# Performance work log

Hardware: AMD Instinct MI355X
Metric: run time of the kernel (lower is better)

## Reference

```python
import jax, jax.numpy as jnp
import numpy as np

N, E, B, D, L, IN, H = 50000, 800000, 64, 64, 4, 7, 4


def _leaky(x, s=0.2):
    return jnp.where(x >= 0, x, s * x)


def _layernorm(x, g, b, eps=1e-5):
    mu = x.mean(-1, keepdims=True)
    v = ((x - mu) ** 2).mean(-1, keepdims=True)
    return (x - mu) * jax.lax.rsqrt(v + eps) * g + b


def _forward(x, edge_index, batch,
             enc_W, enc_b,
             gat_Wl, gat_Wr, gat_att, gat_b,
             ln_g, ln_b, ffn_W1, ffn_b1, ffn_W2, ffn_b2,
             n2g_W1, n2g_b1, n2g_W2, n2g_b2,
             g2n_W1, g2n_b1, g2n_W2, g2n_b2,
             dec_W1, dec_b1, dec_W2, dec_b2):
    n = x.shape[0]
    loops = jnp.arange(n, dtype=edge_index.dtype)
    src = jnp.concatenate([edge_index[0], loops])  # PyG add_self_loops=True
    dst = jnp.concatenate([edge_index[1], loops])

    h = x @ enc_W + enc_b  # encoder [N, D]
    for l in range(L):
        # ---- GATv2Conv(heads=4, concat=False), eval mode (dropout off) ----
        xl = (h @ gat_Wl[l]).reshape(n, H, D)  # source transform (lin_l)
        xr = (h @ gat_Wr[l]).reshape(n, H, D)  # target transform (lin_r)
        s = xl[src] + xr[dst]                              # [Et, H, D]
        e = jnp.sum(_leaky(s) * gat_att[l], axis=-1)       # [Et, H]
        m = jax.ops.segment_max(e, dst, num_segments=n)
        a = jnp.exp(e - m[dst])
        denom = jax.ops.segment_sum(a, dst, num_segments=n)
        a = a / (denom[dst] + 1e-16)                       # segment softmax
        out = jax.ops.segment_sum(a[..., None] * xl[src], dst, num_segments=n)
        out = out.mean(axis=1) + gat_b[l]                  # head average + bias
        # ---- residual + LayerNorm + FFN ----
        h2 = _layernorm(h + out, ln_g[l], ln_b[l])
        h = h2 + (_leaky(h2 @ ffn_W1[l] + ffn_b1[l]) @ ffn_W2[l] + ffn_b2[l])
        # ---- GlobalContextLayer ----
        lat = jax.nn.gelu(h @ n2g_W1[l] + n2g_b1[l]) @ n2g_W2[l] + n2g_b2[l]
        cnt = jax.ops.segment_sum(jnp.ones((n, 1), h.dtype), batch, num_segments=B)
        gmean = jax.ops.segment_sum(lat, batch, num_segments=B) / jnp.maximum(cnt, 1.0)
        gmax = jax.ops.segment_max(lat, batch, num_segments=B)
        gl = jnp.concatenate([gmean, gmax], axis=1)        # [B, 2D]
        ctx = jax.nn.gelu(gl @ g2n_W1[l] + g2n_b1[l]) @ g2n_W2[l] + g2n_b2[l]
        h = h + ctx[batch]
    return jax.nn.gelu(h @ dec_W1 + dec_b1) @ dec_W2 + dec_b2  # [N, 2]


def setup_inputs() -> dict:
    key = jax.random.key(0)
    ks = jax.random.split(key, 16)
    f = lambda i, s: jax.random.normal(ks[i], s, dtype=jnp.float32) * 0.1
    z = lambda s: jnp.zeros(s, jnp.float32)
    return dict(
        x=jax.random.normal(ks[0], (N, IN), dtype=jnp.float32),
        edge_index=jax.random.randint(ks[1], (2, E), 0, N, dtype=jnp.int32),
        batch=jnp.sort(jax.random.randint(ks[2], (N,), 0, B, dtype=jnp.int32)),
        enc_W=f(3, (IN, D)), enc_b=z((D,)),
        gat_Wl=f(4, (L, D, H * D)), gat_Wr=f(5, (L, D, H * D)),
        gat_att=f(6, (L, H, D)), gat_b=z((L, D)),
        ln_g=jnp.ones((L, D), jnp.float32), ln_b=z((L, D)),
        ffn_W1=f(7, (L, D, 2 * D)), ffn_b1=z((L, 2 * D)),
        ffn_W2=f(8, (L, 2 * D, D)), ffn_b2=z((L, D)),
        n2g_W1=f(9, (L, D, D)), n2g_b1=z((L, D)),
        n2g_W2=f(10, (L, D, D)), n2g_b2=z((L, D)),
        g2n_W1=f(11, (L, 2 * D, D)), g2n_b1=z((L, D)),
        g2n_W2=f(12, (L, D, D)), g2n_b2=z((L, D)),
        dec_W1=f(13, (D, D)), dec_b1=z((D,)),
        dec_W2=f(14, (D, 2)), dec_b2=z((2,)),
    )


def reference(x, edge_index, batch, enc_W, enc_b, gat_Wl, gat_Wr, gat_att, gat_b,
              ln_g, ln_b, ffn_W1, ffn_b1, ffn_W2, ffn_b2,
              n2g_W1, n2g_b1, n2g_W2, n2g_b2,
              g2n_W1, g2n_b1, g2n_W2, g2n_b2,
              dec_W1, dec_b1, dec_W2, dec_b2):
    return _forward(x, edge_index, batch, enc_W, enc_b, gat_Wl, gat_Wr, gat_att, gat_b,
                    ln_g, ln_b, ffn_W1, ffn_b1, ffn_W2, ffn_b2,
                    n2g_W1, n2g_b1, n2g_W2, n2g_b2,
                    g2n_W1, g2n_b1, g2n_W2, g2n_b2,
                    dec_W1, dec_b1, dec_W2, dec_b2)
```

## Files before the change

### kernel.cpp

```cpp
#include <hip/hip_runtime.h>
#include <hip/hip_bf16.h>
#include <math.h>

#define NN 50000
#define EE 800000
#define BBATCH 64
#define DDIM 64
#define NLAYER 4
#define NIN 7
#define NHEAD 4

typedef __attribute__((ext_vector_type(8))) short short8v;
typedef __attribute__((ext_vector_type(4))) float f32x4;

static __device__ __forceinline__ float wave_sum(float v) {
#pragma unroll
  for (int m = 32; m > 0; m >>= 1) v += __shfl_xor(v, m, 64);
  return v;
}

static __device__ __forceinline__ float gelu_t(float x) {
  float z = 0.7978845608f * (x + 0.044715f * x * x * x);
  float t = 2.f / (1.f + __expf(-2.f * z)) - 1.f;
  return 0.5f * x * (1.f + t);
}

static __device__ __forceinline__ unsigned short f2b(float v) {
  __hip_bfloat16 b = __float2bfloat16(v);
  return *reinterpret_cast<unsigned short*>(&b);
}

static __device__ __forceinline__ float b2f(unsigned short u) {
  return __builtin_bit_cast(float, (unsigned int)u << 16);
}

template <int CTRL>
static __device__ __forceinline__ float dppf(float v) {
  int x = __builtin_amdgcn_mov_dpp(__builtin_bit_cast(int, v), CTRL, 0xF, 0xF, true);
  return __builtin_bit_cast(float, x);
}

static __device__ __forceinline__ void unpack8(uint4 u, float* xs) {
  unsigned int w[4] = {u.x, u.y, u.z, u.w};
#pragma unroll
  for (int k = 0; k < 4; k++) {
    xs[2 * k]     = __builtin_bit_cast(float, w[k] << 16);
    xs[2 * k + 1] = __builtin_bit_cast(float, w[k] & 0xFFFF0000u);
  }
}

__global__ void k_init_cnt(int* cnt, int n) {
  int i = blockIdx.x * blockDim.x + threadIdx.x;
  if (i < n) cnt[i] = 1;
}

__global__ void k_count_edges(const int* __restrict__ dst, int e, int* cnt) {
  int i = blockIdx.x * blockDim.x + threadIdx.x;
  if (i < e) atomicAdd(&cnt[dst[i]], 1);
}

__global__ void k_scan_bsum(const int* __restrict__ cnt, int n, int* bsum) {
  __shared__ int red[256];
  int b = blockIdx.x, t = threadIdx.x;
  int s = 0;
  for (int i = b * 1024 + t; i < (b + 1) * 1024; i += 256)
    if (i < n) s += cnt[i];
  red[t] = s;
  __syncthreads();
  for (int o = 128; o > 0; o >>= 1) {
    if (t < o) red[t] += red[t + o];
    __syncthreads();
  }
  if (t == 0) bsum[b] = red[0];
}

__global__ void k_scan_offsets(int* bsum, int nb) {
  if (threadIdx.x == 0 && blockIdx.x == 0) {
    int acc = 0;
    for (int i = 0; i < nb; i++) { int v = bsum[i]; bsum[i] = acc; acc += v; }
  }
}

__global__ void k_scan_final(const int* __restrict__ cnt, int n,
                             const int* __restrict__ bsum, int* indptr) {
  __shared__ int lds[256];
  int b = blockIdx.x, t = threadIdx.x;
  int base = b * 1024;
  int v[4];
  int s = 0;
#pragma unroll
  for (int j = 0; j < 4; j++) {
    int i = base + t * 4 + j;
    v[j] = (i < n) ? cnt[i] : 0;
    s += v[j];
  }
  lds[t] = s;
  __syncthreads();
  for (int o = 1; o < 256; o <<= 1) {
    int x = (t >= o) ? lds[t - o] : 0;
    __syncthreads();
    lds[t] += x;
    __syncthreads();
  }
  int run = bsum[b] + lds[t] - s;
#pragma unroll
  for (int j = 0; j < 4; j++) {
    int i = base + t * 4 + j;
    if (i <= n) indptr[i] = run;
    run += v[j];
  }
}

__global__ void k_csr_self(const int* __restrict__ indptr, int* nxt, int* esrc, int n) {
  int i = blockIdx.x * blockDim.x + threadIdx.x;
  if (i < n) {
    int p = indptr[i];
    esrc[p] = i;
    nxt[i] = p + 1;
  }
}

__global__ void k_csr_fill(const int* __restrict__ src, const int* __restrict__ dst,
                           int e, int* nxt, int* esrc) {
  int i = blockIdx.x * blockDim.x + threadIdx.x;
  if (i < e) {
    int p = atomicAdd(&nxt[dst[i]], 1);
    esrc[p] = src[i];
  }
}

__global__ void k_batch_starts(const int* __restrict__ batch, int n, int nb, int* starts) {
  int i = blockIdx.x * blockDim.x + threadIdx.x;
  if (i >= n) return;
  int b = batch[i];
  if (i == 0) {
    for (int x = 0; x <= b; x++) starts[x] = 0;
  } else {
    int pb = batch[i - 1];
    if (pb != b)
      for (int x = pb + 1; x <= b; x++) starts[x] = i;
  }
  if (i == n - 1) {
    for (int x = b + 1; x <= nb; x++) starts[x] = n;
  }
}

#define SEG_LR (4 * 512 * 64)
#define SEG_F1 (4 * 128 * 64)
#define SEG_F2 (4 * 64 * 128)
#define SEG_N  (4 * 64 * 64)
#define SEG_D  (64 * 64)
#define WPREP_TOTAL (SEG_LR + SEG_F1 + SEG_F2 + 2 * SEG_N + SEG_D)
__global__ void k_wprep_all(const float* __restrict__ Wl, const float* __restrict__ Wr,
                            const float* __restrict__ F1, const float* __restrict__ F2,
                            const float* __restrict__ N1, const float* __restrict__ N2,
                            const float* __restrict__ D1,
                            unsigned short* __restrict__ wLR, unsigned short* __restrict__ wF1,
                            unsigned short* __restrict__ wF2, unsigned short* __restrict__ wN1,
                            unsigned short* __restrict__ wN2, unsigned short* __restrict__ wD1) {
  int idx = blockIdx.x * blockDim.x + threadIdx.x;
  if (idx < SEG_LR) {
    int l = idx / (512 * 64), rem = idx % (512 * 64);
    int c = rem / 64, k = rem % 64;
    float v = (c < 256) ? Wl[(size_t)l * 64 * 256 + k * 256 + c]
                        : Wr[(size_t)l * 64 * 256 + k * 256 + (c - 256)];
    wLR[idx] = f2b(v);
    return;
  }
  idx -= SEG_LR;
  if (idx < SEG_F1) {
    int l = idx / (128 * 64), rem = idx % (128 * 64);
    int c = rem / 64, k = rem % 64;
    wF1[idx] = f2b(F1[(size_t)l * 64 * 128 + k * 128 + c]);
    return;
  }
  idx -= SEG_F1;
  if (idx < SEG_F2) {
    int l = idx / (64 * 128), rem = idx % (64 * 128);
    int c = rem / 128, k = rem % 128;
    wF2[idx] = f2b(F2[(size_t)l * 128 * 64 + k * 64 + c]);
    return;
  }
  idx -= SEG_F2;
  if (idx < SEG_N) {
    int l = idx / (64 * 64), rem = idx % (64 * 64);
    int c = rem / 64, k = rem % 64;
    wN1[idx] = f2b(N1[(size_t)l * 64 * 64 + k * 64 + c]);
    return;
  }
  idx -= SEG_N;
  if (idx < SEG_N) {
    int l = idx / (64 * 64), rem = idx % (64 * 64);
    int c = rem / 64, k = rem % 64;
    wN2[idx] = f2b(N2[(size_t)l * 64 * 64 + k * 64 + c]);
    return;
  }
  idx -= SEG_N;
  if (idx < SEG_D) {
    int c = idx / 64, k = idx % 64;
    wD1[idx] = f2b(D1[k * 64 + c]);
  }
}

__global__ void k_encoder(const float* __restrict__ x, const float* __restrict__ W,
                          const float* __restrict__ bias, float* __restrict__ h,
                          unsigned short* __restrict__ hb, int n) {
  int idx = blockIdx.x * blockDim.x + threadIdx.x;
  if (idx >= n * 64) return;
  int i = idx >> 6, d = idx & 63;
  float acc = bias[d];
#pragma unroll
  for (int k = 0; k < NIN; k++) acc += x[i * NIN + k] * W[k * 64 + d];
  h[idx] = acc;
  hb[idx] = f2b(acc);
}

template <int K, int ACT, bool RES, bool BIAS, bool OUTF, bool OUTB>
__global__ __launch_bounds__(256) void k_mgemm(const unsigned short* __restrict__ A,
                                               const unsigned short* __restrict__ Wt,
                                               const float* __restrict__ bias,
                                               const float* __restrict__ res,
                                               float* __restrict__ C,
                                               unsigned short* __restrict__ Cb,
                                               int n, int Co) {
  constexpr int NF = K / 32;
  const int lane = threadIdx.x & 63, wave = threadIdx.x >> 6;
  const int row0 = blockIdx.x * 64 + wave * 16;
  const int c0 = blockIdx.y * 64;
  const int karow = (lane >> 4) * 8;
  const int arow = row0 + (lane & 15);
  const size_t abase = (size_t)(arow < n ? arow : 0) * K + karow;

  short8v a[NF];
#pragma unroll
  for (int f = 0; f < NF; f++)
    a[f] = *(const short8v*)(A + abase + f * 32);

  f32x4 acc[4];
#pragma unroll
  for (int cc = 0; cc < 4; cc++) {
    const int c = c0 + cc * 16 + (lane & 15);
    f32x4 t = {0.f, 0.f, 0.f, 0.f};
#pragma unroll
    for (int f = 0; f < NF; f++) {
      short8v b = *(const short8v*)(Wt + (size_t)c * K + f * 32 + karow);
      t = __builtin_amdgcn_mfma_f32_16x16x32_bf16(a[f], b, t, 0, 0, 0);
    }
    acc[cc] = t;
  }

#pragma unroll
  for (int cc = 0; cc < 4; cc++) {
    const int c = c0 + cc * 16 + (lane & 15);
    const float bv = BIAS ? bias[c] : 0.f;
#pragma unroll
    for (int r = 0; r < 4; r++) {
      const int row = row0 + (lane >> 4) * 4 + r;
      if (row < n) {
        float v = acc[cc][r] + bv;
        if (ACT == 1) v = fmaxf(v, 0.2f * v);
        else if (ACT == 2) v = gelu_t(v);
        if (RES) v += res[(size_t)row * Co + c];
        if (OUTF) C[(size_t)row * Co + c] = v;
        if (OUTB) Cb[(size_t)row * Co + c] = f2b(v);
      }
    }
  }
}

__global__ __launch_bounds__(256) void k_gat(const unsigned short* __restrict__ xlr,
                                             const float* __restrict__ att,
                                             const float* __restrict__ gbias,
                                             const float* __restrict__ lng,
                                             const float* __restrict__ lnb,
                                             const float* __restrict__ h,
                                             const int* __restrict__ indptr,
                                             const int* __restrict__ esrc,
                                             float* __restrict__ h2,
                                             unsigned short* __restrict__ h2b, int n) {
  const int wave = threadIdx.x >> 6, lane = threadIdx.x & 63;
  const int node = blockIdx.x * 4 + wave;
  if (node >= n) return;
  const int q = lane >> 4, r = lane & 15;
  const int c = r & 3;
  const int doff = (r >> 2) * 64 + c * 16;

  float xr_d[16], att_d[16];
  {
    const uint4* xp = (const uint4*)(xlr + (size_t)node * 512 + 256 + doff);
    uint4 u0 = xp[0], u1 = xp[1];
    unpack8(u0, xr_d);
    unpack8(u1, xr_d + 8);
    const float4* ap = (const float4*)(att + doff);
#pragma unroll
    for (int k = 0; k < 4; k++) {
      float4 a = ap[k];
      att_d[4 * k] = a.x; att_d[4 * k + 1] = a.y;
      att_d[4 * k + 2] = a.z; att_d[4 * k + 3] = a.w;
    }
  }

  float acc[16] = {};
  float den = 0.f;
  const int beg = indptr[node], end = indptr[node + 1];

  int j0 = beg + q;
  bool valid = j0 < end;
  {
    int s0 = esrc[valid ? j0 : beg];
    const uint4* xp0 = (const uint4*)(xlr + (size_t)s0 * 512 + doff);
    uint4 u0 = xp0[0], u1 = xp0[1];

    for (int jb = beg; jb < end; jb += 4) {
      const uint4 cu0 = u0, cu1 = u1;
      const bool cvalid = valid;
      if (jb + 4 < end) {
        const int jn = jb + 4 + q;
        valid = jn < end;
        int sn = esrc[valid ? jn : beg];
        const uint4* xpn = (const uint4*)(xlr + (size_t)sn * 512 + doff);
        u0 = xpn[0];
        u1 = xpn[1];
      }
      float xs[16];
      unpack8(cu0, xs);
      unpack8(cu1, xs + 8);
      float p0 = 0.f, p1 = 0.f, p2 = 0.f, p3 = 0.f;
#pragma unroll
      for (int k = 0; k < 4; k++) {
        float t0 = xs[4 * k + 0] + xr_d[4 * k + 0]; t0 = fmaxf(t0, 0.2f * t0); p0 = fmaf(t0, att_d[4 * k + 0], p0);
        float t1 = xs[4 * k + 1] + xr_d[4 * k + 1]; t1 = fmaxf(t1, 0.2f * t1); p1 = fmaf(t1, att_d[4 * k + 1], p1);
        float t2 = xs[4 * k + 2] + xr_d[4 * k + 2]; t2 = fmaxf(t2, 0.2f * t2); p2 = fmaf(t2, att_d[4 * k + 2], p2);
        float t3 = xs[4 * k + 3] + xr_d[4 * k + 3]; t3 = fmaxf(t3, 0.2f * t3); p3 = fmaf(t3, att_d[4 * k + 3], p3);
      }
      float p = (p0 + p1) + (p2 + p3);
      p += dppf<0xB1>(p);
      p += dppf<0x4E>(p);
      const float pw = cvalid ? __expf(fminf(p, 60.f)) : 0.f;
      den += pw;
#pragma unroll
      for (int d = 0; d < 16; d++) acc[d] = fmaf(pw, xs[d], acc[d]);
    }
  }

  den += __shfl_xor(den, 16, 64);
  den += __shfl_xor(den, 32, 64);
#pragma unroll
  for (int d = 0; d < 16; d++) {
    acc[d] += __shfl_xor(acc[d], 16, 64);
    acc[d] += __shfl_xor(acc[d], 32, 64);
  }

  const float rden = 0.25f / (den + 1e-16f);
  float y[16];
  float s4 = 0.f;
  const float4* hp = (const float4*)(h + (size_t)node * 64 + c * 16);
  const float4* gp = (const float4*)(gbias + c * 16);
#pragma unroll
  for (int k = 0; k < 4; k++) {
    float4 hv = hp[k], gv = gp[k];
    float hf[4] = {hv.x, hv.y, hv.z, hv.w};
    float gf[4] = {gv.x, gv.y, gv.z, gv.w};
#pragma unroll
    for (int d2 = 0; d2 < 4; d2++) {
      int d = 4 * k + d2;
      float v = acc[d] * rden;
      v += dppf<0x124>(v);
      v += dppf<0x128>(v);
      y[d] = hf[d2] + v + gf[d2];
      s4 += y[d];
    }
  }

  const float mu = wave_sum(s4) * (1.f / 1024.f);
  float v4 = 0.f;
  float dv[16];
#pragma unroll
  for (int d = 0; d < 16; d++) {
    dv[d] = y[d] - mu;
    v4 += dv[d] * dv[d];
  }
  const float var = wave_sum(v4) * (1.f / 1024.f);
  const float rstd = rsqrtf(var + 1e-5f);

  if (lane < 4) {
    float4* outp = (float4*)(h2 + (size_t)node * 64 + lane * 16);
    uint2* outb = (uint2*)(h2b + (size_t)node * 64 + lane * 16);
    const float4* lgp = (const float4*)(lng + lane * 16);
    const float4* lbp = (const float4*)(lnb + lane * 16);
#pragma unroll
    for (int k = 0; k < 4; k++) {
      float4 g = lgp[k], b = lbp[k];
      float o0 = dv[4 * k + 0] * rstd * g.x + b.x;
      float o1 = dv[4 * k + 1] * rstd * g.y + b.y;
      float o2 = dv[4 * k + 2] * rstd * g.z + b.z;
      float o3 = dv[4 * k + 3] * rstd * g.w + b.w;
      float4 of; of.x = o0; of.y = o1; of.z = o2; of.w = o3;
      outp[k] = of;
      uint2 pk;
      pk.x = (unsigned int)f2b(o0) | ((unsigned int)f2b(o1) << 16);
      pk.y = (unsigned int)f2b(o2) | ((unsigned int)f2b(o3) << 16);
      outb[k] = pk;
    }
  }
}

__global__ void k_pool_part(const float* __restrict__ lat, const int* __restrict__ starts,
                            float* __restrict__ psum, float* __restrict__ pmax) {
  int b = blockIdx.x, p = blockIdx.y;
  int t = threadIdx.x;
  int lane = t & 63, sub = t >> 6;
  int s = starts[b], e = starts[b + 1];
  float sum = 0.f, mx = -3.4e38f;
  for (int i = s + p * 4 + sub; i < e; i += 32) {
    float v = lat[(size_t)i * 64 + lane];
    sum += v;
    mx = fmaxf(mx, v);
  }
  __shared__ float ls[4][64], lm[4][64];
  ls[sub][lane] = sum;
  lm[sub][lane] = mx;
  __syncthreads();
  if (sub == 0) {
#pragma unroll
    for (int j = 1; j < 4; j++) {
      sum += ls[j][lane];
      mx = fmaxf(mx, lm[j][lane]);
    }
    psum[(b * 8 + p) * 64 + lane] = sum;
    pmax[(b * 8 + p) * 64 + lane] = mx;
  }
}

__global__ void k_ctx2(const float* __restrict__ psum, const float* __restrict__ pmax,
                       const int* __restrict__ starts,
                       const float* __restrict__ W1, const float* __restrict__ b1,
                       const float* __restrict__ W2, const float* __restrict__ b2,
                       float* __restrict__ ctx) {
  int b = blockIdx.x;
  int t = threadIdx.x;
  __shared__ float g[128], tt[64];
  int cnt = starts[b + 1] - starts[b];
  if (t < 64) {
    float sm = 0.f;
#pragma unroll
    for (int p = 0; p < 8; p++) sm += psum[(b * 8 + p) * 64 + t];
    g[t] = sm / fmaxf((float)cnt, 1.0f);
  } else {
    float mx = -3.4e38f;
#pragma unroll
    for (int p = 0; p < 8; p++) mx = fmaxf(mx, pmax[(b * 8 + p) * 64 + (t - 64)]);
    g[t] = mx;
  }
  __syncthreads();
  if (t < 64) {
    float acc = b1[t];
    for (int k = 0; k < 128; k++) acc += g[k] * W1[k * 64 + t];
    tt[t] = gelu_t(acc);
  }
  __syncthreads();
  if (t < 64) {
    float acc2 = b2[t];
    for (int k = 0; k < 64; k++) acc2 += tt[k] * W2[k * 64 + t];
    ctx[b * 64 + t] = acc2;
  }
}

__global__ void k_add_ctx(float* __restrict__ h, unsigned short* __restrict__ hb,
                          const float* __restrict__ ctx,
                          const int* __restrict__ batch, int n) {
  int idx = blockIdx.x * blockDim.x + threadIdx.x;
  if (idx >= n * 64) return;
  int i = idx >> 6, d = idx & 63;
  float v = h[idx] + ctx[batch[i] * 64 + d];
  h[idx] = v;
  hb[idx] = f2b(v);
}

__global__ void k_dec2(const unsigned short* __restrict__ tD, const float* __restrict__ W2,
                       const float* __restrict__ b2, float* __restrict__ out, int n) {
  int i = blockIdx.x * blockDim.x + threadIdx.x;
  if (i >= n) return;
  const uint4* rp = (const uint4*)(tD + (size_t)i * 64);
  float a0 = b2[0], a1 = b2[1];
#pragma unroll
  for (int cblk = 0; cblk < 8; cblk++) {
    uint4 u = rp[cblk];
    float xs[8];
    unpack8(u, xs);
#pragma unroll
    for (int d = 0; d < 8; d++) {
      int k = cblk * 8 + d;
      a0 = fmaf(xs[d], W2[k * 2 + 0], a0);
      a1 = fmaf(xs[d], W2[k * 2 + 1], a1);
    }
  }
  out[2 * i] = a0;
  out[2 * i + 1] = a1;
}

extern "C" void kernel_launch(void* const* d_in, const int* in_sizes, int n_in,
                              void* d_out, int out_size, void* d_ws, size_t ws_size,
                              hipStream_t stream) {
  const float* x = (const float*)d_in[0];
  const int* ei = (const int*)d_in[1];
  const int* batch = (const int*)d_in[2];
  const float* enc_W = (const float*)d_in[3];
  const float* enc_b = (const float*)d_in[4];
  const float* gat_Wl = (const float*)d_in[5];
  const float* gat_Wr = (const float*)d_in[6];
  const float* gat_att = (const float*)d_in[7];
  const float* gat_b = (const float*)d_in[8];
  const float* ln_g = (const float*)d_in[9];
  const float* ln_b = (const float*)d_in[10];
  const float* ffn_W1 = (const float*)d_in[11];
  const float* ffn_b1 = (const float*)d_in[12];
  const float* ffn_W2 = (const float*)d_in[13];
  const float* ffn_b2 = (const float*)d_in[14];
  const float* n2g_W1 = (const float*)d_in[15];
  const float* n2g_b1 = (const float*)d_in[16];
  const float* n2g_W2 = (const float*)d_in[17];
  const float* n2g_b2 = (const float*)d_in[18];
  const float* g2n_W1 = (const float*)d_in[19];
  const float* g2n_b1 = (const float*)d_in[20];
  const float* g2n_W2 = (const float*)d_in[21];
  const float* g2n_b2 = (const float*)d_in[22];
  const float* dec_W1 = (const float*)d_in[23];
  const float* dec_b1 = (const float*)d_in[24];
  const float* dec_W2 = (const float*)d_in[25];
  const float* dec_b2 = (const float*)d_in[26];

  const int N = NN, E = EE;
  const int* e_src = ei;
  const int* e_dst = ei + E;

  float* h = (float*)d_ws;
  float* h2 = h + (size_t)N * 64;
  float* t1 = h2 + (size_t)N * 64;
  float* ctx = t1 + (size_t)N * 128;
  float* psum = ctx + BBATCH * 64;
  float* pmax = psum + BBATCH * 8 * 64;
  int* cnt = (int*)(pmax + BBATCH * 8 * 64);
  int* indptr = cnt + N;
  int* esrc = indptr + N + 1;
  int* bsum = esrc + (E + N);
  int* starts = bsum + 64;
  size_t off = (size_t)(starts + BBATCH + 1) - (size_t)d_ws;
  off = (off + 15) & ~(size_t)15;
  unsigned short* hb = (unsigned short*)((char*)d_ws + off);
  unsigned short* h2b = hb + (size_t)N * 64;
  unsigned short* tb = h2b + (size_t)N * 64;
  unsigned short* xlr = tb + (size_t)N * 128;
  unsigned short* wLR = xlr + (size_t)N * 512;
  unsigned short* wF1 = wLR + SEG_LR;
  unsigned short* wF2 = wF1 + SEG_F1;
  unsigned short* wN1 = wF2 + SEG_F2;
  unsigned short* wN2 = wN1 + SEG_N;
  unsigned short* wD1 = wN2 + SEG_N;

  float* lat = t1 + (size_t)N * 64;

  const int TPB = 256;
  const int NBLK_SCAN = (N + 1 + 1023) / 1024;

  hipLaunchKernelGGL(k_wprep_all, dim3((WPREP_TOTAL + 255) / 256), dim3(256), 0, stream,
                     gat_Wl, gat_Wr, ffn_W1, ffn_W2, n2g_W1, n2g_W2, dec_W1,
                     wLR, wF1, wF2, wN1, wN2, wD1);

  hipLaunchKernelGGL(k_init_cnt, dim3((N + TPB - 1) / TPB), dim3(TPB), 0, stream, cnt, N);
  hipLaunchKernelGGL(k_count_edges, dim3((E + TPB - 1) / TPB), dim3(TPB), 0, stream, e_dst, E, cnt);
  hipLaunchKernelGGL(k_scan_bsum, dim3(NBLK_SCAN), dim3(256), 0, stream, cnt, N, bsum);
  hipLaunchKernelGGL(k_scan_offsets, dim3(1), dim3(64), 0, stream, bsum, NBLK_SCAN);
  hipLaunchKernelGGL(k_scan_final, dim3(NBLK_SCAN), dim3(256), 0, stream, cnt, N, bsum, indptr);
  hipLaunchKernelGGL(k_csr_self, dim3((N + TPB - 1) / TPB), dim3(TPB), 0, stream, indptr, cnt, esrc, N);
  hipLaunchKernelGGL(k_csr_fill, dim3((E + TPB - 1) / TPB), dim3(TPB), 0, stream, e_src, e_dst, E, cnt, esrc);
  hipLaunchKernelGGL(k_batch_starts, dim3((N + TPB - 1) / TPB), dim3(TPB), 0, stream, batch, N, BBATCH, starts);

  hipLaunchKernelGGL(k_encoder, dim3((N * 64 + TPB - 1) / TPB), dim3(TPB), 0, stream,
                     x, enc_W, enc_b, h, hb, N);

  const int GN = (N + 63) / 64;

  for (int l = 0; l < NLAYER; l++) {
    const unsigned short* LRt = wLR + (size_t)l * 512 * 64;
    const unsigned short* F1t = wF1 + (size_t)l * 128 * 64;
    const unsigned short* F2t = wF2 + (size_t)l * 64 * 128;
    const unsigned short* N1t = wN1 + (size_t)l * 64 * 64;
    const unsigned short* N2t = wN2 + (size_t)l * 64 * 64;
    const float* attl = gat_att + (size_t)l * 256;
    const float* gbl = gat_b + (size_t)l * 64;
    const float* lngl = ln_g + (size_t)l * 64;
    const float* lnbl = ln_b + (size_t)l * 64;
    const float* fb1 = ffn_b1 + (size_t)l * 128;
    const float* fb2 = ffn_b2 + (size_t)l * 64;
    const float* nb1 = n2g_b1 + (size_t)l * 64;
    const float* nb2 = n2g_b2 + (size_t)l * 64;
    const float* gW1 = g2n_W1 + (size_t)l * 128 * 64;
    const float* gb1 = g2n_b1 + (size_t)l * 64;
    const float* gW2 = g2n_W2 + (size_t)l * 64 * 64;
    const float* gb2 = g2n_b2 + (size_t)l * 64;

    hipLaunchKernelGGL((k_mgemm<64, 0, false, false, false, true>), dim3(GN, 8), dim3(256), 0, stream,
                       hb, LRt, nullptr, nullptr, nullptr, xlr, N, 512);
    hipLaunchKernelGGL(k_gat, dim3((N + 3) / 4), dim3(256), 0, stream,
                       xlr, attl, gbl, lngl, lnbl, h, indptr, esrc, h2, h2b, N);
    hipLaunchKernelGGL((k_mgemm<64, 1, false, true, false, true>), dim3(GN, 2), dim3(256), 0, stream,
                       h2b, F1t, fb1, nullptr, nullptr, tb, N, 128);
    hipLaunchKernelGGL((k_mgemm<128, 0, true, true, true, true>), dim3(GN, 1), dim3(256), 0, stream,
                       tb, F2t, fb2, h2, h, hb, N, 64);
    hipLaunchKernelGGL((k_mgemm<64, 2, false, true, false, true>), dim3(GN, 1), dim3(256), 0, stream,
                       hb, N1t, nb1, nullptr, nullptr, tb, N, 64);
    hipLaunchKernelGGL((k_mgemm<64, 0, false, true, true, false>), dim3(GN, 1), dim3(256), 0, stream,
                       tb, N2t, nb2, nullptr, lat, nullptr, N, 64);
    hipLaunchKernelGGL(k_pool_part, dim3(BBATCH, 8), dim3(256), 0, stream,
                       lat, starts, psum, pmax);
    hipLaunchKernelGGL(k_ctx2, dim3(BBATCH), dim3(128), 0, stream,
                       psum, pmax, starts, gW1, gb1, gW2, gb2, ctx);
    hipLaunchKernelGGL(k_add_ctx, dim3((N * 64 + TPB - 1) / TPB), dim3(TPB), 0, stream,
                       h, hb, ctx, batch, N);
  }

  hipLaunchKernelGGL((k_mgemm<64, 2, false, true, false, true>), dim3(GN, 1), dim3(256), 0, stream,
                     hb, wD1, dec_b1, nullptr, nullptr, tb, N, 64);
  hipLaunchKernelGGL(k_dec2, dim3((N + TPB - 1) / TPB), dim3(TPB), 0, stream,
                     tb, dec_W2, dec_b2, (float*)d_out, N);
}
```

Baseline: 943.4 us.

## Fuse FFN, node-to-graph MLP with pooling, and decoder into single MFMA kernels

```diff
diff --git a/kernel.cpp b/kernel.cpp
--- a/kernel.cpp
+++ b/kernel.cpp
@@ -30,8 +30,13 @@
   return *reinterpret_cast<unsigned short*>(&b);
 }
 
-static __device__ __forceinline__ float b2f(unsigned short u) {
-  return __builtin_bit_cast(float, (unsigned int)u << 16);
+static __device__ __forceinline__ unsigned fkey(float x) {
+  unsigned u = __builtin_bit_cast(unsigned, x);
+  return (u >> 31) ? ~u : (u | 0x80000000u);
+}
+static __device__ __forceinline__ float fkey_inv(unsigned k) {
+  unsigned u = (k & 0x80000000u) ? (k ^ 0x80000000u) : ~k;
+  return __builtin_bit_cast(float, u);
 }
 
 template <int CTRL>
@@ -268,6 +273,152 @@
   }
 }
 
+__global__ __launch_bounds__(256) void k_ffn(const unsigned short* __restrict__ A,
+                                             const unsigned short* __restrict__ W1t,
+                                             const float* __restrict__ b1,
+                                             const unsigned short* __restrict__ W2t,
+                                             const float* __restrict__ b2,
+                                             const float* __restrict__ res,
+                                             float* __restrict__ C,
+                                             unsigned short* __restrict__ Cb, int n) {
+  __shared__ unsigned short tl[4][16 * 136];
+  const int lane = threadIdx.x & 63, wave = threadIdx.x >> 6;
+  const int row0 = blockIdx.x * 64 + wave * 16;
+  const int karow = (lane >> 4) * 8;
+  const int arow = row0 + (lane & 15);
+  const size_t abase = (size_t)(arow < n ? arow : 0) * 64 + karow;
+  short8v a0 = *(const short8v*)(A + abase);
+  short8v a1 = *(const short8v*)(A + abase + 32);
+
+#pragma unroll
+  for (int cc = 0; cc < 8; cc++) {
+    const int c = cc * 16 + (lane & 15);
+    f32x4 t = {0.f, 0.f, 0.f, 0.f};
+    t = __builtin_amdgcn_mfma_f32_16x16x32_bf16(a0, *(const short8v*)(W1t + (size_t)c * 64 + karow), t, 0, 0, 0);
+    t = __builtin_amdgcn_mfma_f32_16x16x32_bf16(a1, *(const short8v*)(W1t + (size_t)c * 64 + 32 + karow), t, 0, 0, 0);
+    const float bv = b1[c];
+#pragma unroll
+    for (int r = 0; r < 4; r++) {
+      float v = t[r] + bv;
+      v = fmaxf(v, 0.2f * v);
+      int rr = (lane >> 4) * 4 + r;
+      tl[wave][rr * 136 + c] = f2b(v);
+    }
+  }
+  __syncthreads();
+
+  short8v a2[4];
+#pragma unroll
+  for (int f = 0; f < 4; f++)
+    a2[f] = *(const short8v*)(&tl[wave][(lane & 15) * 136 + f * 32 + karow]);
+
+#pragma unroll
+  for (int cc = 0; cc < 4; cc++) {
+    const int c = cc * 16 + (lane & 15);
+    f32x4 t = {0.f, 0.f, 0.f, 0.f};
+#pragma unroll
+    for (int f = 0; f < 4; f++)
+      t = __builtin_amdgcn_mfma_f32_16x16x32_bf16(a2[f], *(const short8v*)(W2t + (size_t)c * 128 + f * 32 + karow), t, 0, 0, 0);
+    const float bv = b2[c];
+#pragma unroll
+    for (int r = 0; r < 4; r++) {
+      const int row = row0 + (lane >> 4) * 4 + r;
+      if (row < n) {
+        float v = t[r] + bv + res[(size_t)row * 64 + c];
+        C[(size_t)row * 64 + c] = v;
+        Cb[(size_t)row * 64 + c] = f2b(v);
+      }
+    }
+  }
+}
+
+__global__ __launch_bounds__(256) void k_n2g(const unsigned short* __restrict__ A,
+                                             const unsigned short* __restrict__ W1t,
+                                             const float* __restrict__ b1,
+                                             const unsigned short* __restrict__ W2t,
+                                             const float* __restrict__ b2,
+                                             const int* __restrict__ batch,
+                                             float* __restrict__ psum,
+                                             unsigned int* __restrict__ pmax, int n) {
+  __shared__ unsigned short tl[4][16 * 72];
+  __shared__ float s_sum[64];
+  __shared__ unsigned s_max[64];
+  const int lane = threadIdx.x & 63, wave = threadIdx.x >> 6;
+  const int row0b = blockIdx.x * 64;
+  const int row0 = row0b + wave * 16;
+  const int karow = (lane >> 4) * 8;
+  const int arow = row0 + (lane & 15);
+  const size_t abase = (size_t)(arow < n ? arow : 0) * 64 + karow;
+  if (threadIdx.x < 64) { s_sum[threadIdx.x] = 0.f; s_max[threadIdx.x] = 0u; }
+  short8v a0 = *(const short8v*)(A + abase);
+  short8v a1 = *(const short8v*)(A + abase + 32);
+
+#pragma unroll
+  for (int cc = 0; cc < 4; cc++) {
+    const int c = cc * 16 + (lane & 15);
+    f32x4 t = {0.f, 0.f, 0.f, 0.f};
+    t = __builtin_amdgcn_mfma_f32_16x16x32_bf16(a0, *(const short8v*)(W1t + (size_t)c * 64 + karow), t, 0, 0, 0);
+    t = __builtin_amdgcn_mfma_f32_16x16x32_bf16(a1, *(const short8v*)(W1t + (size_t)c * 64 + 32 + karow), t, 0, 0, 0);
+    const float bv = b1[c];
+#pragma unroll
+    for (int r = 0; r < 4; r++) {
+      int rr = (lane >> 4) * 4 + r;
+      tl[wave][rr * 72 + c] = f2b(gelu_t(t[r] + bv));
+    }
+  }
+  __syncthreads();
+
+  short8v a2[2];
+#pragma unroll
+  for (int f = 0; f < 2; f++)
+    a2[f] = *(const short8v*)(&tl[wave][(lane & 15) * 72 + f * 32 + karow]);
+
+  float pv[4][4];
+#pragma unroll
+  for (int cc = 0; cc < 4; cc++) {
+    const int c = cc * 16 + (lane & 15);
+    f32x4 t = {0.f, 0.f, 0.f, 0.f};
+    t = __builtin_amdgcn_mfma_f32_16x16x32_bf16(a2[0], *(const short8v*)(W2t + (size_t)c * 64 + karow), t, 0, 0, 0);
+    t = __builtin_amdgcn_mfma_f32_16x16x32_bf16(a2[1], *(const short8v*)(W2t + (size_t)c * 64 + 32 + karow), t, 0, 0, 0);
+    const float bv = b2[c];
+#pragma unroll
+    for (int r = 0; r < 4; r++) pv[cc][r] = t[r] + bv;
+  }
+
+  const int blo = batch[row0b];
+  const int last = row0b + 63 < n ? row0b + 63 : n - 1;
+  const int bhi = batch[last];
+  if (blo == bhi && row0b + 63 < n) {
+#pragma unroll
+    for (int cc = 0; cc < 4; cc++) {
+      const int c = cc * 16 + (lane & 15);
+      float s = pv[cc][0] + pv[cc][1] + pv[cc][2] + pv[cc][3];
+      float mx = fmaxf(fmaxf(pv[cc][0], pv[cc][1]), fmaxf(pv[cc][2], pv[cc][3]));
+      atomicAdd(&s_sum[c], s);
+      atomicMax(&s_max[c], fkey(mx));
+    }
+    __syncthreads();
+    if (threadIdx.x < 64) {
+      atomicAdd(&psum[blo * 64 + threadIdx.x], s_sum[threadIdx.x]);
+      atomicMax(&pmax[blo * 64 + threadIdx.x], s_max[threadIdx.x]);
+    }
+  } else {
+#pragma unroll
+    for (int cc = 0; cc < 4; cc++) {
+      const int c = cc * 16 + (lane & 15);
+#pragma unroll
+      for (int r = 0; r < 4; r++) {
+        const int row = row0 + (lane >> 4) * 4 + r;
+        if (row < n) {
+          const int b = batch[row];
+          atomicAdd(&psum[b * 64 + c], pv[cc][r]);
+          atomicMax(&pmax[b * 64 + c], fkey(pv[cc][r]));
+        }
+      }
+    }
+  }
+}
+
 __global__ __launch_bounds__(256) void k_gat(const unsigned short* __restrict__ xlr,
                                              const float* __restrict__ att,
                                              const float* __restrict__ gbias,
@@ -305,42 +456,42 @@
   const int beg = indptr[node], end = indptr[node + 1];
 
   int j0 = beg + q;
-  bool valid = j0 < end;
-  {
-    int s0 = esrc[valid ? j0 : beg];
-    const uint4* xp0 = (const uint4*)(xlr + (size_t)s0 * 512 + doff);
-    uint4 u0 = xp0[0], u1 = xp0[1];
-
-    for (int jb = beg; jb < end; jb += 4) {
-      const uint4 cu0 = u0, cu1 = u1;
-      const bool cvalid = valid;
-      if (jb + 4 < end) {
-        const int jn = jb + 4 + q;
-        valid = jn < end;
-        int sn = esrc[valid ? jn : beg];
-        const uint4* xpn = (const uint4*)(xlr + (size_t)sn * 512 + doff);
-        u0 = xpn[0];
-        u1 = xpn[1];
+  int s_cur = esrc[(j0 < end) ? j0 : beg];
+  const uint4* xp0 = (const uint4*)(xlr + (size_t)s_cur * 512 + doff);
+  uint4 u0 = xp0[0], u1 = xp0[1];
+  int jn1 = beg + 4 + q;
+  int s_nxt = esrc[(jn1 < end && beg + 4 < end) ? jn1 : beg];
+
+  for (int jb = beg; jb < end; jb += 4) {
+    const uint4 cu0 = u0, cu1 = u1;
+    const bool cvalid = (jb + q) < end;
+    if (jb + 4 < end) {
+      const uint4* xpn = (const uint4*)(xlr + (size_t)s_nxt * 512 + doff);
+      u0 = xpn[0];
+      u1 = xpn[1];
+      if (jb + 8 < end) {
+        const int jn = jb + 8 + q;
+        s_nxt = esrc[(jn < end) ? jn : beg];
       }
-      float xs[16];
-      unpack8(cu0, xs);
-      unpack8(cu1, xs + 8);
-      float p0 = 0.f, p1 = 0.f, p2 = 0.f, p3 = 0.f;
-#pragma unroll
-      for (int k = 0; k < 4; k++) {
-        float t0 = xs[4 * k + 0] + xr_d[4 * k + 0]; t0 = fmaxf(t0, 0.2f * t0); p0 = fmaf(t0, att_d[4 * k + 0], p0);
-        float t1 = xs[4 * k + 1] + xr_d[4 * k + 1]; t1 = fmaxf(t1, 0.2f * t1); p1 = fmaf(t1, att_d[4 * k + 1], p1);
-        float t2 = xs[4 * k + 2] + xr_d[4 * k + 2]; t2 = fmaxf(t2, 0.2f * t2); p2 = fmaf(t2, att_d[4 * k + 2], p2);
-        float t3 = xs[4 * k + 3] + xr_d[4 * k + 3]; t3 = fmaxf(t3, 0.2f * t3); p3 = fmaf(t3, att_d[4 * k + 3], p3);
-      }
-      float p = (p0 + p1) + (p2 + p3);
-      p += dppf<0xB1>(p);
-      p += dppf<0x4E>(p);
-      const float pw = cvalid ? __expf(fminf(p, 60.f)) : 0.f;
-      den += pw;
-#pragma unroll
-      for (int d = 0; d < 16; d++) acc[d] = fmaf(pw, xs[d], acc[d]);
-    }
+    }
+    float xs[16];
+    unpack8(cu0, xs);
+    unpack8(cu1, xs + 8);
+    float p0 = 0.f, p1 = 0.f, p2 = 0.f, p3 = 0.f;
+#pragma unroll
+    for (int k = 0; k < 4; k++) {
+      float t0 = xs[4 * k + 0] + xr_d[4 * k + 0]; t0 = fmaxf(t0, 0.2f * t0); p0 = fmaf(t0, att_d[4 * k + 0], p0);
+      float t1 = xs[4 * k + 1] + xr_d[4 * k + 1]; t1 = fmaxf(t1, 0.2f * t1); p1 = fmaf(t1, att_d[4 * k + 1], p1);
+      float t2 = xs[4 * k + 2] + xr_d[4 * k + 2]; t2 = fmaxf(t2, 0.2f * t2); p2 = fmaf(t2, att_d[4 * k + 2], p2);
+      float t3 = xs[4 * k + 3] + xr_d[4 * k + 3]; t3 = fmaxf(t3, 0.2f * t3); p3 = fmaf(t3, att_d[4 * k + 3], p3);
+    }
+    float p = (p0 + p1) + (p2 + p3);
+    p += dppf<0xB1>(p);
+    p += dppf<0x4E>(p);
+    const float pw = cvalid ? __expf(fminf(p, 60.f)) : 0.f;
+    den += pw;
+#pragma unroll
+    for (int d = 0; d < 16; d++) acc[d] = fmaf(pw, xs[d], acc[d]);
   }
 
   den += __shfl_xor(den, 16, 64);
@@ -405,34 +556,7 @@
   }
 }
 
-__global__ void k_pool_part(const float* __restrict__ lat, const int* __restrict__ starts,
-                            float* __restrict__ psum, float* __restrict__ pmax) {
-  int b = blockIdx.x, p = blockIdx.y;
-  int t = threadIdx.x;
-  int lane = t & 63, sub = t >> 6;
-  int s = starts[b], e = starts[b + 1];
-  float sum = 0.f, mx = -3.4e38f;
-  for (int i = s + p * 4 + sub; i < e; i += 32) {
-    float v = lat[(size_t)i * 64 + lane];
-    sum += v;
-    mx = fmaxf(mx, v);
-  }
-  __shared__ float ls[4][64], lm[4][64];
-  ls[sub][lane] = sum;
-  lm[sub][lane] = mx;
-  __syncthreads();
-  if (sub == 0) {
-#pragma unroll
-    for (int j = 1; j < 4; j++) {
-      sum += ls[j][lane];
-      mx = fmaxf(mx, lm[j][lane]);
-    }
-    psum[(b * 8 + p) * 64 + lane] = sum;
-    pmax[(b * 8 + p) * 64 + lane] = mx;
-  }
-}
-
-__global__ void k_ctx2(const float* __restrict__ psum, const float* __restrict__ pmax,
+__global__ void k_ctx2(const float* __restrict__ psum, const unsigned int* __restrict__ pmax,
                        const int* __restrict__ starts,
                        const float* __restrict__ W1, const float* __restrict__ b1,
                        const float* __restrict__ W2, const float* __restrict__ b2,
@@ -442,15 +566,9 @@
   __shared__ float g[128], tt[64];
   int cnt = starts[b + 1] - starts[b];
   if (t < 64) {
-    float sm = 0.f;
-#pragma unroll
-    for (int p = 0; p < 8; p++) sm += psum[(b * 8 + p) * 64 + t];
-    g[t] = sm / fmaxf((float)cnt, 1.0f);
+    g[t] = psum[b * 64 + t] / fmaxf((float)cnt, 1.0f);
   } else {
-    float mx = -3.4e38f;
-#pragma unroll
-    for (int p = 0; p < 8; p++) mx = fmaxf(mx, pmax[(b * 8 + p) * 64 + (t - 64)]);
-    g[t] = mx;
+    g[t] = fkey_inv(pmax[b * 64 + (t - 64)]);
   }
   __syncthreads();
   if (t < 64) {
@@ -477,26 +595,54 @@
   hb[idx] = f2b(v);
 }
 
-__global__ void k_dec2(const unsigned short* __restrict__ tD, const float* __restrict__ W2,
-                       const float* __restrict__ b2, float* __restrict__ out, int n) {
-  int i = blockIdx.x * blockDim.x + threadIdx.x;
-  if (i >= n) return;
-  const uint4* rp = (const uint4*)(tD + (size_t)i * 64);
-  float a0 = b2[0], a1 = b2[1];
-#pragma unroll
-  for (int cblk = 0; cblk < 8; cblk++) {
-    uint4 u = rp[cblk];
-    float xs[8];
-    unpack8(u, xs);
-#pragma unroll
-    for (int d = 0; d < 8; d++) {
-      int k = cblk * 8 + d;
-      a0 = fmaf(xs[d], W2[k * 2 + 0], a0);
-      a1 = fmaf(xs[d], W2[k * 2 + 1], a1);
-    }
-  }
-  out[2 * i] = a0;
-  out[2 * i + 1] = a1;
+__global__ __launch_bounds__(256) void k_dec(const unsigned short* __restrict__ A,
+                                             const unsigned short* __restrict__ W1t,
+                                             const float* __restrict__ b1,
+                                             const float* __restrict__ W2,
+                                             const float* __restrict__ b2,
+                                             float* __restrict__ out, int n) {
+  const int lane = threadIdx.x & 63, wave = threadIdx.x >> 6;
+  const int row0 = blockIdx.x * 64 + wave * 16;
+  const int karow = (lane >> 4) * 8;
+  const int arow = row0 + (lane & 15);
+  const size_t abase = (size_t)(arow < n ? arow : 0) * 64 + karow;
+  short8v a0 = *(const short8v*)(A + abase);
+  short8v a1 = *(const short8v*)(A + abase + 32);
+
+  float o0[4] = {}, o1[4] = {};
+#pragma unroll
+  for (int cc = 0; cc < 4; cc++) {
+    const int cidx = cc * 16 + (lane & 15);
+    f32x4 t = {0.f, 0.f, 0.f, 0.f};
+    t = __builtin_amdgcn_mfma_f32_16x16x32_bf16(a0, *(const short8v*)(W1t + (size_t)cidx * 64 + karow), t, 0, 0, 0);
+    t = __builtin_amdgcn_mfma_f32_16x16x32_bf16(a1, *(const short8v*)(W1t + (size_t)cidx * 64 + 32 + karow), t, 0, 0, 0);
+    const float bv = b1[cidx];
+    const float w0 = W2[cidx * 2 + 0], w1 = W2[cidx * 2 + 1];
+#pragma unroll
+    for (int r = 0; r < 4; r++) {
+      float v = gelu_t(t[r] + bv);
+      o0[r] = fmaf(v, w0, o0[r]);
+      o1[r] = fmaf(v, w1, o1[r]);
+    }
+  }
+#pragma unroll
+  for (int m = 1; m < 16; m <<= 1) {
+#pragma unroll
+    for (int r = 0; r < 4; r++) {
+      o0[r] += __shfl_xor(o0[r], m, 64);
+      o1[r] += __shfl_xor(o1[r], m, 64);
+    }
+  }
+  if ((lane & 15) == 0) {
+#pragma unroll
+    for (int r = 0; r < 4; r++) {
+      const int row = row0 + (lane >> 4) * 4 + r;
+      if (row < n) {
+        out[2 * row] = o0[r] + b2[0];
+        out[2 * row + 1] = o1[r] + b2[1];
+      }
+    }
+  }
 }
 
 extern "C" void kernel_launch(void* const* d_in, const int* in_sizes, int n_in,
@@ -536,11 +682,10 @@
 
   float* h = (float*)d_ws;
   float* h2 = h + (size_t)N * 64;
-  float* t1 = h2 + (size_t)N * 64;
-  float* ctx = t1 + (size_t)N * 128;
+  float* ctx = h2 + (size_t)N * 64;
   float* psum = ctx + BBATCH * 64;
-  float* pmax = psum + BBATCH * 8 * 64;
-  int* cnt = (int*)(pmax + BBATCH * 8 * 64);
+  unsigned int* pmax = (unsigned int*)(psum + BBATCH * 64);
+  int* cnt = (int*)(pmax + BBATCH * 64);
   int* indptr = cnt + N;
   int* esrc = indptr + N + 1;
   int* bsum = esrc + (E + N);
@@ -549,16 +694,13 @@
   off = (off + 15) & ~(size_t)15;
   unsigned short* hb = (unsigned short*)((char*)d_ws + off);
   unsigned short* h2b = hb + (size_t)N * 64;
-  unsigned short* tb = h2b + (size_t)N * 64;
-  unsigned short* xlr = tb + (size_t)N * 128;
+  unsigned short* xlr = h2b + (size_t)N * 64;
   unsigned short* wLR = xlr + (size_t)N * 512;
   unsigned short* wF1 = wLR + SEG_LR;
   unsigned short* wF2 = wF1 + SEG_F1;
   unsigned short* wN1 = wF2 + SEG_F2;
   unsigned short* wN2 = wN1 + SEG_N;
   unsigned short* wD1 = wN2 + SEG_N;
-
-  float* lat = t1 + (size_t)N * 64;
 
   const int TPB = 256;
   const int NBLK_SCAN = (N + 1 + 1023) / 1024;
@@ -604,24 +746,17 @@
                        hb, LRt, nullptr, nullptr, nullptr, xlr, N, 512);
     hipLaunchKernelGGL(k_gat, dim3((N + 3) / 4), dim3(256), 0, stream,
                        xlr, attl, gbl, lngl, lnbl, h, indptr, esrc, h2, h2b, N);
-    hipLaunchKernelGGL((k_mgemm<64, 1, false, true, false, true>), dim3(GN, 2), dim3(256), 0, stream,
-                       h2b, F1t, fb1, nullptr, nullptr, tb, N, 128);
-    hipLaunchKernelGGL((k_mgemm<128, 0, true, true, true, true>), dim3(GN, 1), dim3(256), 0, stream,
-                       tb, F2t, fb2, h2, h, hb, N, 64);
-    hipLaunchKernelGGL((k_mgemm<64, 2, false, true, false, true>), dim3(GN, 1), dim3(256), 0, stream,
-                       hb, N1t, nb1, nullptr, nullptr, tb, N, 64);
-    hipLaunchKernelGGL((k_mgemm<64, 0, false, true, true, false>), dim3(GN, 1), dim3(256), 0, stream,
-                       tb, N2t, nb2, nullptr, lat, nullptr, N, 64);
-    hipLaunchKernelGGL(k_pool_part, dim3(BBATCH, 8), dim3(256), 0, stream,
-                       lat, starts, psum, pmax);
+    hipLaunchKernelGGL(k_ffn, dim3(GN), dim3(256), 0, stream,
+                       h2b, F1t, fb1, F2t, fb2, h2, h, hb, N);
+    hipMemsetAsync(psum, 0, BBATCH * 64 * (sizeof(float) + sizeof(unsigned int)), stream);
+    hipLaunchKernelGGL(k_n2g, dim3(GN), dim3(256), 0, stream,
+                       hb, N1t, nb1, N2t, nb2, batch, psum, pmax, N);
     hipLaunchKernelGGL(k_ctx2, dim3(BBATCH), dim3(128), 0, stream,
                        psum, pmax, starts, gW1, gb1, gW2, gb2, ctx);
     hipLaunchKernelGGL(k_add_ctx, dim3((N * 64 + TPB - 1) / TPB), dim3(TPB), 0, stream,
                        h, hb, ctx, batch, N);
   }
 
-  hipLaunchKernelGGL((k_mgemm<64, 2, false, true, false, true>), dim3(GN, 1), dim3(256), 0, stream,
-                     hb, wD1, dec_b1, nullptr, nullptr, tb, N, 64);
-  hipLaunchKernelGGL(k_dec2, dim3((N + TPB - 1) / TPB), dim3(TPB), 0, stream,
-                     tb, dec_W2, dec_b2, (float*)d_out, N);
-}
+  hipLaunchKernelGGL(k_dec, dim3(GN), dim3(256), 0, stream,
+                     hb, wD1, dec_b1, dec_W2, dec_b2, (float*)d_out, N);
+}
```

Result: faster. 869.4 us (-7.8%).
